# Optimization experiments

Measured on AMD Instinct MI355X. Metric: run time of the kernel, lower is better.

Reference implementation:

```python
import jax, jax.numpy as jnp
import numpy as np

H = 2048      # hidden_size
C = 256       # controller_hidden
B = 8192      # batch (tokens)
DT = 0.1


def setup_inputs() -> dict:
    key = jax.random.key(0)
    ks = jax.random.split(key, 8)
    h = jax.random.normal(ks[0], (B, H), dtype=jnp.float32)
    v = jax.random.normal(ks[1], (B, H), dtype=jnp.float32)
    # controller_in: Linear(2H -> C)
    W_in = jax.random.normal(ks[2], (C, 2 * H), dtype=jnp.float32) / np.sqrt(2 * H)
    b_in = jax.random.normal(ks[3], (C,), dtype=jnp.float32) * 0.01
    # controller_out: Linear(C -> 3H), weight ~ N(0, 0.01); bias init [2.2, -2.2, 0.0] per split
    W_out = jax.random.normal(ks[4], (3 * H, C), dtype=jnp.float32) * 0.01
    b_out = jnp.concatenate([
        jnp.full((H,), 2.2, dtype=jnp.float32),
        jnp.full((H,), -2.2, dtype=jnp.float32),
        jnp.zeros((H,), dtype=jnp.float32),
    ])
    # mu_proj: Linear(H -> H, bias=False); init zeros in module, use small random for a non-trivial baseline
    W_mu = jax.random.normal(ks[5], (H, H), dtype=jnp.float32) * 0.01
    mu = jnp.zeros((H,), dtype=jnp.float32)
    return {"h": h, "v": v, "W_in": W_in, "b_in": b_in, "W_out": W_out,
            "b_out": b_out, "W_mu": W_mu, "mu": mu}


def reference(h, v, W_in, b_in, W_out, b_out, W_mu, mu):
    hv = jnp.concatenate([h, v], axis=-1)                    # [B, 2H]
    ctrl = jax.nn.silu(hv @ W_in.T + b_in)                   # [B, C]
    ctrl_out = ctrl @ W_out.T + b_out                        # [B, 3H]
    alpha_raw, beta_raw, gate_raw = jnp.split(ctrl_out, 3, axis=-1)
    alpha = jax.nn.sigmoid(alpha_raw)
    beta = jnp.minimum(jax.nn.softplus(beta_raw), 2.0)
    gate = jax.nn.sigmoid(gate_raw)
    mu_contextual = mu + h @ W_mu.T                          # [B, H]
    error = h - mu_contextual
    v_next = jnp.clip(alpha * v - beta * error, -10.0, 10.0)
    h_next = h + DT * gate * v_next
    return h_next, v_next, mu_contextual
```

## Files before the change

### kernel.cpp

```cpp
#include <hip/hip_runtime.h>
#include <cstdint>
#include <cstddef>

#define B_TOK 8192
#define HDIM  2048
#define CDIM  256
#define KHV   4096
#define N3H   6144
#define DT_C  0.1f

typedef __bf16 bf16x8 __attribute__((ext_vector_type(8)));
typedef float  f32x4  __attribute__((ext_vector_type(4)));

typedef __attribute__((address_space(1))) void as1_void;
typedef __attribute__((address_space(3))) void as3_void;

#define VM_WAIT(N) asm volatile("s_waitcnt vmcnt(" #N ")" ::: "memory")
#define SCHED_FENCE() __builtin_amdgcn_sched_barrier(0)

__device__ __forceinline__ void g2l16(const void* g, void* l) {
    __builtin_amdgcn_global_load_lds((as1_void*)(void*)(uintptr_t)(g),
                                     (as3_void*)l, 16, 0, 0);
}

__device__ __forceinline__ unsigned short f2bf(float f) {
    unsigned int u = __float_as_uint(f);
    u += 0x7fffu + ((u >> 16) & 1u);
    return (unsigned short)(u >> 16);
}

__device__ __forceinline__ float bf2f(unsigned short s) {
    return __uint_as_float((unsigned int)s << 16);
}

__device__ __forceinline__ float fsigmoid(float x) {
    return __builtin_amdgcn_rcpf(1.f + __expf(-x));
}
__device__ __forceinline__ float fsoftplus(float x) {
    float t = __expf(-fabsf(x));
    return fmaxf(x, 0.f) + 0.69314718056f * __log2f(1.f + t);
}

__global__ void k_convert(const float* __restrict__ hp, const float* __restrict__ vp,
                          const float* __restrict__ Win, const float* __restrict__ Wout,
                          const float* __restrict__ Wmu,
                          ushort4* __restrict__ hv_b, ushort4* __restrict__ Wmu_b,
                          ushort4* __restrict__ Wout_b, ushort4* __restrict__ Win_b)
{
    const int HV_V   = B_TOK * KHV / 4;
    const int WMU_V  = HDIM * HDIM / 4;
    const int WOUT_V = N3H * CDIM / 4;
    const int WIN_V  = CDIM * KHV / 4;
    const int TOT    = HV_V + WMU_V + WOUT_V + WIN_V;
    for (int i = blockIdx.x * blockDim.x + threadIdx.x; i < TOT;
         i += gridDim.x * blockDim.x) {
        float4 x;
        ushort4* dst;
        if (i < HV_V) {
            int b  = i >> 10;
            int c4 = i & 1023;
            x = (c4 < 512) ? ((const float4*)hp)[b * 512 + c4]
                           : ((const float4*)vp)[b * 512 + (c4 - 512)];
            dst = hv_b + i;
        } else if (i < HV_V + WMU_V) {
            int j = i - HV_V;
            x = ((const float4*)Wmu)[j];
            dst = Wmu_b + j;
        } else if (i < HV_V + WMU_V + WOUT_V) {
            int j = i - (HV_V + WMU_V);
            x = ((const float4*)Wout)[j];
            dst = Wout_b + j;
        } else {
            int j = i - (HV_V + WMU_V + WOUT_V);
            x = ((const float4*)Win)[j];
            dst = Win_b + j;
        }
        ushort4 o;
        o.x = __builtin_bit_cast(unsigned short, (__bf16)x.x);
        o.y = __builtin_bit_cast(unsigned short, (__bf16)x.y);
        o.z = __builtin_bit_cast(unsigned short, (__bf16)x.z);
        o.w = __builtin_bit_cast(unsigned short, (__bf16)x.w);
        *dst = o;
    }
}

__global__ __launch_bounds__(256, 2)
void k_mid(const unsigned short* __restrict__ hvb,
           const unsigned short* __restrict__ Winb,
           const unsigned short* __restrict__ Wmub,
           const float* __restrict__ b_in,
           const float* __restrict__ mu,
           unsigned short* __restrict__ ctrl,
           float* __restrict__ outmu)
{
    __shared__ unsigned short sA[2][4096];
    __shared__ unsigned short sB[2][4096];
    const int tid  = threadIdx.x;
    const int wid  = tid >> 6;
    const int lane = tid & 63;
    const int quad = lane >> 4;
    const int l15  = lane & 15;
    const int wm   = wid >> 1, wn = wid & 1;
    const int srow = lane >> 2;
    const int sk   = (lane & 3) * 8;

    if (blockIdx.x < 512) {
        const int s  = ((int)blockIdx.x & 7) * 64 + ((int)blockIdx.x >> 3);
        const int bm = (s >> 2) * 64;
        const int bn = (s & 3) * 64;

        f32x4 acc[2][2];
#pragma unroll
        for (int a = 0; a < 2; ++a)
#pragma unroll
            for (int b = 0; b < 2; ++b) acc[a][b] = (f32x4){0.f, 0.f, 0.f, 0.f};

        const unsigned short* Ag = hvb  + (size_t)(bm + wid * 16 + srow) * KHV + sk;
        const unsigned short* Bg = Winb + (size_t)(bn + wid * 16 + srow) * KHV + sk;

        auto stage = [&](int cb, int t) {
            g2l16(Ag + t * 32, &sA[cb][(wid * 16) * 32]);
            g2l16(Bg + t * 32, &sB[cb][(wid * 16) * 32]);
        };
        auto compute = [&](int cb) {
            bf16x8 aF[2], bF[2];
#pragma unroll
            for (int t = 0; t < 2; ++t)
                aF[t] = *(const bf16x8*)&sA[cb][(wm * 32 + t * 16 + l15) * 32 + quad * 8];
#pragma unroll
            for (int t = 0; t < 2; ++t)
                bF[t] = *(const bf16x8*)&sB[cb][(wn * 32 + t * 16 + l15) * 32 + quad * 8];
#pragma unroll
            for (int tm = 0; tm < 2; ++tm)
#pragma unroll
                for (int tn = 0; tn < 2; ++tn)
                    acc[tm][tn] = __builtin_amdgcn_mfma_f32_16x16x32_bf16(
                        aF[tm], bF[tn], acc[tm][tn], 0, 0, 0);
        };

        const int nt = KHV / 32;
        stage(0, 0);
        stage(1, 1);
        for (int t = 0; t < nt - 1; ++t) {
            VM_WAIT(2);
            __builtin_amdgcn_s_barrier();
            SCHED_FENCE();
            compute(t & 1);
            SCHED_FENCE();
            __builtin_amdgcn_s_barrier();
            SCHED_FENCE();
            if (t + 2 < nt) stage(t & 1, t + 2);
        }
        VM_WAIT(0);
        __builtin_amdgcn_s_barrier();
        SCHED_FENCE();
        compute((nt - 1) & 1);

#pragma unroll
        for (int tm = 0; tm < 2; ++tm)
#pragma unroll
            for (int tn = 0; tn < 2; ++tn) {
                const int n = bn + wn * 32 + tn * 16 + l15;
                const float bias = b_in[n];
#pragma unroll
                for (int r = 0; r < 4; ++r) {
                    const int m = bm + wm * 32 + tm * 16 + quad * 4 + r;
                    float x = acc[tm][tn][r] + bias;
                    float s2 = x * fsigmoid(x);
                    ctrl[(size_t)m * CDIM + n] = f2bf(s2);
                }
            }
    } else {
        const int t3  = (int)blockIdx.x - 512;
        const int t3s = (t3 & 7) * 128 + (t3 >> 3);
        const int bm  = (t3s & 63) * 128;
        const int bn  = (t3s >> 6) * 128;

        f32x4 acc[4][4];
#pragma unroll
        for (int a = 0; a < 4; ++a)
#pragma unroll
            for (int b = 0; b < 4; ++b) acc[a][b] = (f32x4){0.f, 0.f, 0.f, 0.f};

        const unsigned short* Ag0 = hvb  + (size_t)(bm + wid * 16 + srow) * KHV + sk;
        const unsigned short* Ag1 = hvb  + (size_t)(bm + (wid + 4) * 16 + srow) * KHV + sk;
        const unsigned short* Bg0 = Wmub + (size_t)(bn + wid * 16 + srow) * HDIM + sk;
        const unsigned short* Bg1 = Wmub + (size_t)(bn + (wid + 4) * 16 + srow) * HDIM + sk;

        auto stage = [&](int cb, int t) {
            g2l16(Ag0 + t * 32, &sA[cb][(wid * 16) * 32]);
            g2l16(Ag1 + t * 32, &sA[cb][((wid + 4) * 16) * 32]);
            g2l16(Bg0 + t * 32, &sB[cb][(wid * 16) * 32]);
            g2l16(Bg1 + t * 32, &sB[cb][((wid + 4) * 16) * 32]);
        };
        auto compute = [&](int cb) {
            bf16x8 aF[4], bF[4];
#pragma unroll
            for (int t = 0; t < 4; ++t)
                aF[t] = *(const bf16x8*)&sA[cb][(wm * 64 + t * 16 + l15) * 32 + quad * 8];
#pragma unroll
            for (int t = 0; t < 4; ++t)
                bF[t] = *(const bf16x8*)&sB[cb][(wn * 64 + t * 16 + l15) * 32 + quad * 8];
#pragma unroll
            for (int tm = 0; tm < 4; ++tm)
#pragma unroll
                for (int tn = 0; tn < 4; ++tn)
                    acc[tm][tn] = __builtin_amdgcn_mfma_f32_16x16x32_bf16(
                        aF[tm], bF[tn], acc[tm][tn], 0, 0, 0);
        };

        const int nt = HDIM / 32;
        stage(0, 0);
        stage(1, 1);
        for (int t = 0; t < nt - 1; ++t) {
            VM_WAIT(4);
            __builtin_amdgcn_s_barrier();
            SCHED_FENCE();
            compute(t & 1);
            SCHED_FENCE();
            __builtin_amdgcn_s_barrier();
            SCHED_FENCE();
            if (t + 2 < nt) stage(t & 1, t + 2);
        }
        VM_WAIT(0);
        __builtin_amdgcn_s_barrier();
        SCHED_FENCE();
        compute((nt - 1) & 1);

#pragma unroll
        for (int tm = 0; tm < 4; ++tm)
#pragma unroll
            for (int tn = 0; tn < 4; ++tn) {
                const int n = bn + wn * 64 + tn * 16 + l15;
                const float mub = mu[n];
#pragma unroll
                for (int r = 0; r < 4; ++r) {
                    const int m = bm + wm * 64 + tm * 16 + quad * 4 + r;
                    outmu[(size_t)m * HDIM + n] = acc[tm][tn][r] + mub;
                }
            }
    }
}

__global__ __launch_bounds__(256, 4)
void k_gemm2(const unsigned short* __restrict__ A,
             const unsigned short* __restrict__ Bw,
             const float* __restrict__ b_out,
             const unsigned short* __restrict__ hv,
             const float* __restrict__ mu_ctx,
             float* __restrict__ outp)
{
    __shared__ unsigned short sA[64 * 32];
    __shared__ unsigned short sB[3][64 * 32];
    const int tid  = threadIdx.x;
    const int wid  = tid >> 6;
    const int lane = tid & 63;
    const int quad = lane >> 4;
    const int l15  = lane & 15;
    const int wm   = wid >> 1, wn = wid & 1;
    const int bm   = blockIdx.x * 64;
    const int bn   = blockIdx.y * 64;
    const int srow = lane >> 2;
    const int sk   = (lane & 3) * 8;

    f32x4 acc[3][2][2];
#pragma unroll
    for (int p = 0; p < 3; ++p)
#pragma unroll
        for (int a = 0; a < 2; ++a)
#pragma unroll
            for (int b = 0; b < 2; ++b) acc[p][a][b] = (f32x4){0.f, 0.f, 0.f, 0.f};

    const unsigned short* Ag  = A + (size_t)(bm + wid * 16 + srow) * CDIM + sk;
    const unsigned short* Bg0 = Bw + (size_t)(0 * HDIM + bn + wid * 16 + srow) * CDIM + sk;
    const unsigned short* Bg1 = Bw + (size_t)(1 * HDIM + bn + wid * 16 + srow) * CDIM + sk;
    const unsigned short* Bg2 = Bw + (size_t)(2 * HDIM + bn + wid * 16 + srow) * CDIM + sk;
    unsigned short* lA  = &sA[(wid * 16) * 32];
    unsigned short* lB0 = &sB[0][(wid * 16) * 32];
    unsigned short* lB1 = &sB[1][(wid * 16) * 32];
    unsigned short* lB2 = &sB[2][(wid * 16) * 32];

    for (int kt = 0; kt < CDIM; kt += 32) {
        g2l16(Ag  + kt, lA);
        g2l16(Bg0 + kt, lB0);
        g2l16(Bg1 + kt, lB1);
        g2l16(Bg2 + kt, lB2);
        __syncthreads();
        bf16x8 aF[2], bF[3][2];
#pragma unroll
        for (int t = 0; t < 2; ++t)
            aF[t] = *(const bf16x8*)&sA[(wm * 32 + t * 16 + l15) * 32 + quad * 8];
#pragma unroll
        for (int p = 0; p < 3; ++p)
#pragma unroll
            for (int t = 0; t < 2; ++t)
                bF[p][t] = *(const bf16x8*)&sB[p][(wn * 32 + t * 16 + l15) * 32 + quad * 8];
#pragma unroll
        for (int p = 0; p < 3; ++p)
#pragma unroll
            for (int tm = 0; tm < 2; ++tm)
#pragma unroll
                for (int tn = 0; tn < 2; ++tn)
                    acc[p][tm][tn] = __builtin_amdgcn_mfma_f32_16x16x32_bf16(
                        aF[tm], bF[p][tn], acc[p][tm][tn], 0, 0, 0);
        __syncthreads();
    }

#pragma unroll
    for (int tm = 0; tm < 2; ++tm)
#pragma unroll
        for (int tn = 0; tn < 2; ++tn) {
            const int i  = bn + wn * 32 + tn * 16 + l15;
            const float ba = b_out[i];
            const float bb = b_out[HDIM + i];
            const float bg = b_out[2 * HDIM + i];
#pragma unroll
            for (int r = 0; r < 4; ++r) {
                const int m = bm + wm * 32 + tm * 16 + quad * 4 + r;
                const size_t off = (size_t)m * HDIM + i;
                const float araw = acc[0][tm][tn][r] + ba;
                const float braw = acc[1][tm][tn][r] + bb;
                const float graw = acc[2][tm][tn][r] + bg;
                const float alpha = fsigmoid(araw);
                const float beta  = fminf(fsoftplus(braw), 2.f);
                const float gate  = fsigmoid(graw);
                const float hh = bf2f(hv[(size_t)m * KHV + i]);
                const float vv = bf2f(hv[(size_t)m * KHV + HDIM + i]);
                const float mm = mu_ctx[off];
                const float err = hh - mm;
                float vn = alpha * vv - beta * err;
                vn = fminf(fmaxf(vn, -10.f), 10.f);
                const float hn = hh + DT_C * gate * vn;
                outp[off] = hn;
                outp[(size_t)B_TOK * HDIM + off] = vn;
            }
        }
}

extern "C" void kernel_launch(void* const* d_in, const int* in_sizes, int n_in,
                              void* d_out, int out_size, void* d_ws, size_t ws_size,
                              hipStream_t stream)
{
    const float* hp    = (const float*)d_in[0];
    const float* vp    = (const float*)d_in[1];
    const float* Win   = (const float*)d_in[2];
    const float* b_in  = (const float*)d_in[3];
    const float* Wout  = (const float*)d_in[4];
    const float* b_out = (const float*)d_in[5];
    const float* Wmu   = (const float*)d_in[6];
    const float* mu    = (const float*)d_in[7];
    float* outp = (float*)d_out;

    char* ws = (char*)d_ws;
    size_t off = 0;
    unsigned short* hv_b   = (unsigned short*)(ws + off); off += (size_t)B_TOK * KHV * 2;
    unsigned short* Wmu_b  = (unsigned short*)(ws + off); off += (size_t)HDIM * HDIM * 2;
    unsigned short* Wout_b = (unsigned short*)(ws + off); off += (size_t)N3H * CDIM * 2;
    unsigned short* Win_b  = (unsigned short*)(ws + off); off += (size_t)CDIM * KHV * 2;
    unsigned short* ctrl   = (unsigned short*)(ws + off); off += (size_t)B_TOK * CDIM * 2;

    k_convert<<<dim3(4096), dim3(256), 0, stream>>>(
        hp, vp, Win, Wout, Wmu,
        (ushort4*)hv_b, (ushort4*)Wmu_b, (ushort4*)Wout_b, (ushort4*)Win_b);

    k_mid<<<dim3(1536), dim3(256), 0, stream>>>(
        hv_b, Win_b, Wmu_b, b_in, mu, ctrl, outp + (size_t)2 * B_TOK * HDIM);

    k_gemm2<<<dim3(128, 32), dim3(256), 0, stream>>>(
        ctrl, Wout_b, b_out, hv_b,
        outp + (size_t)2 * B_TOK * HDIM, outp);
}
```

Measured before the change: 516.5 us.

## Enlarge mu GEMM tiles, interleave GEMM1/mu blocks, double-buffer gemm2 K loop

The mu-projection GEMM tile grows from 128x128 to 256x128, halving its block count to 512. Its blocks are now interleaved with the controller-input GEMM blocks in groups of 8, and both share one pooled LDS buffer. The output GEMM k_gemm2 gains a two-stage double-buffered global-to-LDS pipeline in place of its load-sync-compute loop. The larger tile raises register pressure (32 accumulator vectors plus 8 A fragments) and LDS use, which may lower occupancy under launch_bounds(256,2).

```diff
diff --git a/kernel.cpp b/kernel.cpp
--- a/kernel.cpp
+++ b/kernel.cpp
@@ -93,8 +93,7 @@
            unsigned short* __restrict__ ctrl,
            float* __restrict__ outmu)
 {
-    __shared__ unsigned short sA[2][4096];
-    __shared__ unsigned short sB[2][4096];
+    __shared__ unsigned short pool[2][12288];
     const int tid  = threadIdx.x;
     const int wid  = tid >> 6;
     const int lane = tid & 63;
@@ -104,8 +103,12 @@
     const int srow = lane >> 2;
     const int sk   = (lane & 3) * 8;
 
-    if (blockIdx.x < 512) {
-        const int s  = ((int)blockIdx.x & 7) * 64 + ((int)blockIdx.x >> 3);
+    const int bidx = (int)blockIdx.x;
+    const int isG1 = ((bidx >> 3) & 1) == 0;
+    const int gidx = (bidx >> 4) * 8 + (bidx & 7);
+
+    if (isG1) {
+        const int s  = (gidx & 7) * 64 + (gidx >> 3);
         const int bm = (s >> 2) * 64;
         const int bn = (s & 3) * 64;
 
@@ -119,17 +122,17 @@
         const unsigned short* Bg = Winb + (size_t)(bn + wid * 16 + srow) * KHV + sk;
 
         auto stage = [&](int cb, int t) {
-            g2l16(Ag + t * 32, &sA[cb][(wid * 16) * 32]);
-            g2l16(Bg + t * 32, &sB[cb][(wid * 16) * 32]);
+            g2l16(Ag + t * 32, &pool[cb][(wid * 16) * 32]);
+            g2l16(Bg + t * 32, &pool[cb][2048 + (wid * 16) * 32]);
         };
         auto compute = [&](int cb) {
             bf16x8 aF[2], bF[2];
 #pragma unroll
             for (int t = 0; t < 2; ++t)
-                aF[t] = *(const bf16x8*)&sA[cb][(wm * 32 + t * 16 + l15) * 32 + quad * 8];
+                aF[t] = *(const bf16x8*)&pool[cb][(wm * 32 + t * 16 + l15) * 32 + quad * 8];
 #pragma unroll
             for (int t = 0; t < 2; ++t)
-                bF[t] = *(const bf16x8*)&sB[cb][(wn * 32 + t * 16 + l15) * 32 + quad * 8];
+                bF[t] = *(const bf16x8*)&pool[cb][2048 + (wn * 32 + t * 16 + l15) * 32 + quad * 8];
 #pragma unroll
             for (int tm = 0; tm < 2; ++tm)
 #pragma unroll
@@ -171,38 +174,39 @@
                 }
             }
     } else {
-        const int t3  = (int)blockIdx.x - 512;
-        const int t3s = (t3 & 7) * 128 + (t3 >> 3);
-        const int bm  = (t3s & 63) * 128;
-        const int bn  = (t3s >> 6) * 128;
-
-        f32x4 acc[4][4];
-#pragma unroll
-        for (int a = 0; a < 4; ++a)
+        const int t3s = (gidx & 7) * 64 + (gidx >> 3);
+        const int bm  = (t3s & 31) * 256;
+        const int bn  = (t3s >> 5) * 128;
+
+        f32x4 acc[8][4];
+#pragma unroll
+        for (int a = 0; a < 8; ++a)
 #pragma unroll
             for (int b = 0; b < 4; ++b) acc[a][b] = (f32x4){0.f, 0.f, 0.f, 0.f};
 
-        const unsigned short* Ag0 = hvb  + (size_t)(bm + wid * 16 + srow) * KHV + sk;
-        const unsigned short* Ag1 = hvb  + (size_t)(bm + (wid + 4) * 16 + srow) * KHV + sk;
-        const unsigned short* Bg0 = Wmub + (size_t)(bn + wid * 16 + srow) * HDIM + sk;
-        const unsigned short* Bg1 = Wmub + (size_t)(bn + (wid + 4) * 16 + srow) * HDIM + sk;
+        const unsigned short* A3 = hvb  + (size_t)(bm + wid * 16 + srow) * KHV + sk;
+        const unsigned short* B3 = Wmub + (size_t)(bn + wid * 16 + srow) * HDIM + sk;
 
         auto stage = [&](int cb, int t) {
-            g2l16(Ag0 + t * 32, &sA[cb][(wid * 16) * 32]);
-            g2l16(Ag1 + t * 32, &sA[cb][((wid + 4) * 16) * 32]);
-            g2l16(Bg0 + t * 32, &sB[cb][(wid * 16) * 32]);
-            g2l16(Bg1 + t * 32, &sB[cb][((wid + 4) * 16) * 32]);
+#pragma unroll
+            for (int r = 0; r < 4; ++r)
+                g2l16(A3 + (size_t)r * 64 * KHV + t * 32,
+                      &pool[cb][(r * 64 + wid * 16) * 32]);
+#pragma unroll
+            for (int r = 0; r < 2; ++r)
+                g2l16(B3 + (size_t)r * 64 * HDIM + t * 32,
+                      &pool[cb][8192 + (r * 64 + wid * 16) * 32]);
         };
         auto compute = [&](int cb) {
-            bf16x8 aF[4], bF[4];
+            bf16x8 aF[8], bF[4];
+#pragma unroll
+            for (int t = 0; t < 8; ++t)
+                aF[t] = *(const bf16x8*)&pool[cb][(wm * 128 + t * 16 + l15) * 32 + quad * 8];
 #pragma unroll
             for (int t = 0; t < 4; ++t)
-                aF[t] = *(const bf16x8*)&sA[cb][(wm * 64 + t * 16 + l15) * 32 + quad * 8];
-#pragma unroll
-            for (int t = 0; t < 4; ++t)
-                bF[t] = *(const bf16x8*)&sB[cb][(wn * 64 + t * 16 + l15) * 32 + quad * 8];
-#pragma unroll
-            for (int tm = 0; tm < 4; ++tm)
+                bF[t] = *(const bf16x8*)&pool[cb][8192 + (wn * 64 + t * 16 + l15) * 32 + quad * 8];
+#pragma unroll
+            for (int tm = 0; tm < 8; ++tm)
 #pragma unroll
                 for (int tn = 0; tn < 4; ++tn)
                     acc[tm][tn] = __builtin_amdgcn_mfma_f32_16x16x32_bf16(
@@ -213,7 +217,7 @@
         stage(0, 0);
         stage(1, 1);
         for (int t = 0; t < nt - 1; ++t) {
-            VM_WAIT(4);
+            VM_WAIT(6);
             __builtin_amdgcn_s_barrier();
             SCHED_FENCE();
             compute(t & 1);
@@ -228,14 +232,14 @@
         compute((nt - 1) & 1);
 
 #pragma unroll
-        for (int tm = 0; tm < 4; ++tm)
+        for (int tm = 0; tm < 8; ++tm)
 #pragma unroll
             for (int tn = 0; tn < 4; ++tn) {
                 const int n = bn + wn * 64 + tn * 16 + l15;
                 const float mub = mu[n];
 #pragma unroll
                 for (int r = 0; r < 4; ++r) {
-                    const int m = bm + wm * 64 + tm * 16 + quad * 4 + r;
+                    const int m = bm + wm * 128 + tm * 16 + quad * 4 + r;
                     outmu[(size_t)m * HDIM + n] = acc[tm][tn][r] + mub;
                 }
             }
@@ -250,8 +254,8 @@
              const float* __restrict__ mu_ctx,
              float* __restrict__ outp)
 {
-    __shared__ unsigned short sA[64 * 32];
-    __shared__ unsigned short sB[3][64 * 32];
+    __shared__ unsigned short sA[2][2048];
+    __shared__ unsigned short sB[2][3][2048];
     const int tid  = threadIdx.x;
     const int wid  = tid >> 6;
     const int lane = tid & 63;
@@ -275,26 +279,23 @@
     const unsigned short* Bg0 = Bw + (size_t)(0 * HDIM + bn + wid * 16 + srow) * CDIM + sk;
     const unsigned short* Bg1 = Bw + (size_t)(1 * HDIM + bn + wid * 16 + srow) * CDIM + sk;
     const unsigned short* Bg2 = Bw + (size_t)(2 * HDIM + bn + wid * 16 + srow) * CDIM + sk;
-    unsigned short* lA  = &sA[(wid * 16) * 32];
-    unsigned short* lB0 = &sB[0][(wid * 16) * 32];
-    unsigned short* lB1 = &sB[1][(wid * 16) * 32];
-    unsigned short* lB2 = &sB[2][(wid * 16) * 32];
-
-    for (int kt = 0; kt < CDIM; kt += 32) {
-        g2l16(Ag  + kt, lA);
-        g2l16(Bg0 + kt, lB0);
-        g2l16(Bg1 + kt, lB1);
-        g2l16(Bg2 + kt, lB2);
-        __syncthreads();
+
+    auto stage = [&](int cb, int t) {
+        g2l16(Ag  + t * 32, &sA[cb][(wid * 16) * 32]);
+        g2l16(Bg0 + t * 32, &sB[cb][0][(wid * 16) * 32]);
+        g2l16(Bg1 + t * 32, &sB[cb][1][(wid * 16) * 32]);
+        g2l16(Bg2 + t * 32, &sB[cb][2][(wid * 16) * 32]);
+    };
+    auto compute = [&](int cb) {
         bf16x8 aF[2], bF[3][2];
 #pragma unroll
         for (int t = 0; t < 2; ++t)
-            aF[t] = *(const bf16x8*)&sA[(wm * 32 + t * 16 + l15) * 32 + quad * 8];
+            aF[t] = *(const bf16x8*)&sA[cb][(wm * 32 + t * 16 + l15) * 32 + quad * 8];
 #pragma unroll
         for (int p = 0; p < 3; ++p)
 #pragma unroll
             for (int t = 0; t < 2; ++t)
-                bF[p][t] = *(const bf16x8*)&sB[p][(wn * 32 + t * 16 + l15) * 32 + quad * 8];
+                bF[p][t] = *(const bf16x8*)&sB[cb][p][(wn * 32 + t * 16 + l15) * 32 + quad * 8];
 #pragma unroll
         for (int p = 0; p < 3; ++p)
 #pragma unroll
@@ -303,8 +304,25 @@
                 for (int tn = 0; tn < 2; ++tn)
                     acc[p][tm][tn] = __builtin_amdgcn_mfma_f32_16x16x32_bf16(
                         aF[tm], bF[p][tn], acc[p][tm][tn], 0, 0, 0);
-        __syncthreads();
+    };
+
+    const int nt = CDIM / 32;
+    stage(0, 0);
+    stage(1, 1);
+    for (int t = 0; t < nt - 1; ++t) {
+        VM_WAIT(4);
+        __builtin_amdgcn_s_barrier();
+        SCHED_FENCE();
+        compute(t & 1);
+        SCHED_FENCE();
+        __builtin_amdgcn_s_barrier();
+        SCHED_FENCE();
+        if (t + 2 < nt) stage(t & 1, t + 2);
     }
+    VM_WAIT(0);
+    __builtin_amdgcn_s_barrier();
+    SCHED_FENCE();
+    compute((nt - 1) & 1);
 
 #pragma unroll
     for (int tm = 0; tm < 2; ++tm)
@@ -363,7 +381,7 @@
         hp, vp, Win, Wout, Wmu,
         (ushort4*)hv_b, (ushort4*)Wmu_b, (ushort4*)Wout_b, (ushort4*)Win_b);
 
-    k_mid<<<dim3(1536), dim3(256), 0, stream>>>(
+    k_mid<<<dim3(1024), dim3(256), 0, stream>>>(
         hv_b, Win_b, Wmu_b, b_in, mu, ctrl, outp + (size_t)2 * B_TOK * HDIM);
 
     k_gemm2<<<dim3(128, 32), dim3(256), 0, stream>>>(
```

Result: no change. 519.3 us (+0.5%).
